# Kernel optimization log

Hardware: AMD Instinct MI355X
Metric: run time of the kernel (lower is better)

Reference implementation:

```python
import jax, jax.numpy as jnp
import numpy as np

N = 4096
E_EDGES = 262144
F_IN = 128      # num_features
H = 4           # nhead (GAT heads and MHA heads)
C = 64          # d_model (per-head GAT out dim)
EMB = H * C     # 256, MHA embed_dim
DFF = 128       # dim_feedforward
HD = EMB // H   # MHA head dim = 64


def setup_inputs() -> dict:
    key = jax.random.key(0)
    ks = jax.random.split(key, 16)
    inp = {}
    inp["tgt"] = jax.random.normal(ks[0], (N, F_IN), jnp.float32)
    inp["memory"] = jax.random.normal(ks[1], (N, EMB), jnp.float32)
    inp["original_signal"] = jax.random.normal(ks[2], (N, EMB), jnp.float32)
    inp["edge_index"] = jax.random.randint(ks[3], (2, E_EDGES), 0, N, jnp.int32)
    # GATConv params (PyG: lin has no bias; separate bias of size H*C; att vectors [1,H,C])
    s = 1.0 / np.sqrt(F_IN)
    inp["W_gat"] = jax.random.normal(ks[4], (F_IN, H * C), jnp.float32) * s
    inp["att_src"] = jax.random.normal(ks[5], (H, C), jnp.float32) * (1.0 / np.sqrt(C))
    inp["att_dst"] = jax.random.normal(ks[6], (H, C), jnp.float32) * (1.0 / np.sqrt(C))
    inp["b_gat"] = jnp.zeros((H * C,), jnp.float32)
    # nn.MultiheadAttention params
    se = 1.0 / np.sqrt(EMB)
    inp["in_proj_w"] = jax.random.normal(ks[7], (3 * EMB, EMB), jnp.float32) * se
    inp["in_proj_b"] = jnp.zeros((3 * EMB,), jnp.float32)
    inp["out_proj_w"] = jax.random.normal(ks[8], (EMB, EMB), jnp.float32) * se
    inp["out_proj_b"] = jnp.zeros((EMB,), jnp.float32)
    # linear1
    inp["lin1_w"] = jax.random.normal(ks[9], (DFF, EMB), jnp.float32) * se
    inp["lin1_b"] = jnp.zeros((DFF,), jnp.float32)
    return inp


def _gat_conv(x, edge_index, W, att_src, att_dst, bias):
    n = x.shape[0]
    xh = (x @ W).reshape(n, H, C)                       # [N,H,C]
    a_s = jnp.sum(xh * att_src, axis=-1)                # [N,H]
    a_d = jnp.sum(xh * att_dst, axis=-1)                # [N,H]
    # add self loops (PyG default add_self_loops=True)
    loop = jnp.arange(n, dtype=edge_index.dtype)
    src = jnp.concatenate([edge_index[0], loop])
    dst = jnp.concatenate([edge_index[1], loop])
    alpha = jax.nn.leaky_relu(a_s[src] + a_d[dst], negative_slope=0.2)  # [E+N,H]
    # edge softmax grouped by destination node
    m = jax.ops.segment_max(alpha, dst, num_segments=n)
    alpha = jnp.exp(alpha - m[dst])
    denom = jax.ops.segment_sum(alpha, dst, num_segments=n)
    alpha = alpha / (denom[dst] + 1e-16)
    # message passing: weighted scatter-add of source features
    out = jax.ops.segment_sum(xh[src] * alpha[:, :, None], dst, num_segments=n)  # [N,H,C]
    return out.reshape(n, H * C) + bias


def _mha(q_in, k_in, v_in, in_proj_w, in_proj_b, out_proj_w, out_proj_b):
    # batch=1, seq=N; dropout inactive (eval)
    q = q_in @ in_proj_w[:EMB].T + in_proj_b[:EMB]
    k = k_in @ in_proj_w[EMB:2 * EMB].T + in_proj_b[EMB:2 * EMB]
    v = v_in @ in_proj_w[2 * EMB:].T + in_proj_b[2 * EMB:]
    q = q.reshape(-1, H, HD)
    k = k.reshape(-1, H, HD)
    v = v.reshape(-1, H, HD)
    scale = 1.0 / np.sqrt(HD)
    scores = jnp.einsum('nhd,mhd->hnm', q * scale, k)   # [H,N,N]
    attn = jax.nn.softmax(scores, axis=-1)
    o = jnp.einsum('hnm,mhd->nhd', attn, v).reshape(-1, EMB)
    return o @ out_proj_w.T + out_proj_b


def reference(tgt, memory, original_signal, edge_index,
              W_gat, att_src, att_dst, b_gat,
              in_proj_w, in_proj_b, out_proj_w, out_proj_b,
              lin1_w, lin1_b):
    t = _gat_conv(tgt, edge_index, W_gat, att_src, att_dst, b_gat)
    t = jax.nn.leaky_relu(t, negative_slope=0.01)       # F.leaky_relu default slope
    fused = _mha(t, memory, original_signal, in_proj_w, in_proj_b, out_proj_w, out_proj_b)
    return jax.nn.relu(fused @ lin1_w.T + lin1_b)       # [N, DFF]
```

## Files before the change

kernel.cpp:

```cpp
#include <hip/hip_runtime.h>
#include <hip/hip_bf16.h>

#define NN   4096
#define EE   262144
#define ET   (EE + NN)
#define HH   4
#define EMB  256
#define DFF  128
#define FIN  128
#define KSPLIT 8
#define KCHUNK (NN / KSPLIT)

typedef float  f32x16  __attribute__((ext_vector_type(16)));
typedef __bf16 bf16x8  __attribute__((ext_vector_type(8)));
typedef unsigned short u16;
typedef unsigned short u16x4 __attribute__((ext_vector_type(4)));

__device__ __forceinline__ u16 f2bf(float f) {
  unsigned u = __float_as_uint(f);
  u += 0x7fffu + ((u >> 16) & 1u);
  return (u16)(u >> 16);
}
__device__ __forceinline__ unsigned split1(float x) {
  const u16 h = f2bf(x);
  const float hf = __uint_as_float(((unsigned)h) << 16);
  const u16 l = f2bf(x - hf);
  return (unsigned)h | ((unsigned)l << 16);
}

__global__ __launch_bounds__(256) void mgemm_nt(
    const float* __restrict__ A, const float* __restrict__ B,
    float* __restrict__ Cf, int M, int Nn, int K)
{
  __shared__ u16 Ah[64][40], Al[64][40], Bh[64][40], Bl[64][40];
  const int tid = threadIdx.x;
  const int m0 = blockIdx.y * 64, n0 = blockIdx.x * 64;
  const int w = tid >> 6, l = tid & 63, lq = l & 31, hi = l >> 5;
  const int wm = w >> 1, wn = w & 1;
  f32x16 acc = {0};
  for (int k0 = 0; k0 < K; k0 += 32) {
    __syncthreads();
#pragma unroll
    for (int it = 0; it < 2; ++it) {
      const int idx = tid + it * 256;
      {
        const int row = idx >> 3, slot = idx & 7;
        const float4 av = *(const float4*)(A + (size_t)(m0 + row) * K + k0 + slot * 4);
        const unsigned s0 = split1(av.x), s1 = split1(av.y), s2 = split1(av.z), s3 = split1(av.w);
        u16x4 hp = {(u16)s0, (u16)s1, (u16)s2, (u16)s3};
        u16x4 lp = {(u16)(s0 >> 16), (u16)(s1 >> 16), (u16)(s2 >> 16), (u16)(s3 >> 16)};
        *(u16x4*)(&Ah[row][slot * 4]) = hp;
        *(u16x4*)(&Al[row][slot * 4]) = lp;
      }
      {
        const int kr = idx >> 4, nq = idx & 15;
        const float4 bv = *(const float4*)(B + (size_t)(k0 + kr) * Nn + n0 + nq * 4);
        const unsigned s0 = split1(bv.x), s1 = split1(bv.y), s2 = split1(bv.z), s3 = split1(bv.w);
        Bh[nq * 4 + 0][kr] = (u16)s0; Bl[nq * 4 + 0][kr] = (u16)(s0 >> 16);
        Bh[nq * 4 + 1][kr] = (u16)s1; Bl[nq * 4 + 1][kr] = (u16)(s1 >> 16);
        Bh[nq * 4 + 2][kr] = (u16)s2; Bl[nq * 4 + 2][kr] = (u16)(s2 >> 16);
        Bh[nq * 4 + 3][kr] = (u16)s3; Bl[nq * 4 + 3][kr] = (u16)(s3 >> 16);
      }
    }
    __syncthreads();
#pragma unroll
    for (int c = 0; c < 2; ++c) {
      const bf16x8 ah = *(const bf16x8*)(&Ah[wm * 32 + lq][c * 16 + hi * 8]);
      const bf16x8 al = *(const bf16x8*)(&Al[wm * 32 + lq][c * 16 + hi * 8]);
      const bf16x8 bh = *(const bf16x8*)(&Bh[wn * 32 + lq][c * 16 + hi * 8]);
      const bf16x8 bl = *(const bf16x8*)(&Bl[wn * 32 + lq][c * 16 + hi * 8]);
      acc = __builtin_amdgcn_mfma_f32_32x32x16_bf16(ah, bh, acc, 0, 0, 0);
      acc = __builtin_amdgcn_mfma_f32_32x32x16_bf16(ah, bl, acc, 0, 0, 0);
      acc = __builtin_amdgcn_mfma_f32_32x32x16_bf16(al, bh, acc, 0, 0, 0);
    }
  }
  const int col = n0 + wn * 32 + lq;
#pragma unroll
  for (int r = 0; r < 16; ++r) {
    const int row = m0 + wm * 32 + (r & 3) + 8 * (r >> 2) + 4 * hi;
    Cf[(size_t)row * Nn + col] = acc[r];
  }
}

__global__ __launch_bounds__(256) void bgemm(
    const float* __restrict__ A, const float* __restrict__ B, const float* __restrict__ bias,
    float* __restrict__ Cf, int M, int Nn, int K, int act)
{
  __shared__ u16 As[64][40], Bs[64][40];
  const int tid = threadIdx.x;
  const int m0 = blockIdx.y * 64, n0 = blockIdx.x * 64;
  const int w = tid >> 6, l = tid & 63, lq = l & 31, hi = l >> 5;
  const int wm = w >> 1, wn = w & 1;
  f32x16 acc = {0};
  for (int k0 = 0; k0 < K; k0 += 32) {
    __syncthreads();
#pragma unroll
    for (int it = 0; it < 2; ++it) {
      const int idx = tid + it * 256;
      const int row = idx >> 3, slot = idx & 7;
      const float4 av = *(const float4*)(A + (size_t)(m0 + row) * K + k0 + slot * 4);
      u16x4 ap = {f2bf(av.x), f2bf(av.y), f2bf(av.z), f2bf(av.w)};
      *(u16x4*)(&As[row][slot * 4]) = ap;
      const float4 bv = *(const float4*)(B + (size_t)(n0 + row) * K + k0 + slot * 4);
      u16x4 bp = {f2bf(bv.x), f2bf(bv.y), f2bf(bv.z), f2bf(bv.w)};
      *(u16x4*)(&Bs[row][slot * 4]) = bp;
    }
    __syncthreads();
#pragma unroll
    for (int c = 0; c < 2; ++c) {
      const bf16x8 af = *(const bf16x8*)(&As[wm * 32 + lq][c * 16 + hi * 8]);
      const bf16x8 bf = *(const bf16x8*)(&Bs[wn * 32 + lq][c * 16 + hi * 8]);
      acc = __builtin_amdgcn_mfma_f32_32x32x16_bf16(af, bf, acc, 0, 0, 0);
    }
  }
  const int col = n0 + wn * 32 + lq;
  const float bcol = bias ? bias[col] : 0.f;
#pragma unroll
  for (int r = 0; r < 16; ++r) {
    const int row = m0 + wm * 32 + (r & 3) + 8 * (r >> 2) + 4 * hi;
    float v = acc[r] + bcol;
    if (act == 2) v = fmaxf(v, 0.f);
    Cf[(size_t)row * Nn + col] = v;
  }
}

__global__ __launch_bounds__(256) void qkv_mfma(
    const float* __restrict__ tbuf, const float* __restrict__ mem, const float* __restrict__ orig,
    const float* __restrict__ ipw, const float* __restrict__ ipb,
    u16* __restrict__ qb, u16* __restrict__ kbuf, u16* __restrict__ vT)
{
  __shared__ u16 As[64][40], Bs[64][40];
  const int z = blockIdx.z;
  const float* A = (z == 0) ? tbuf : (z == 1 ? mem : orig);
  const float* B = ipw + (size_t)z * EMB * EMB;
  const float* bias = ipb + z * EMB;
  const float oscale = (z == 0) ? 0.125f : 1.f;
  const int tid = threadIdx.x;
  const int m0 = blockIdx.y * 64, n0 = blockIdx.x * 64;
  const int w = tid >> 6, l = tid & 63, lq = l & 31, hi = l >> 5;
  const int wm = w >> 1, wn = w & 1;
  f32x16 acc = {0};
  for (int k0 = 0; k0 < EMB; k0 += 32) {
    __syncthreads();
#pragma unroll
    for (int it = 0; it < 2; ++it) {
      const int idx = tid + it * 256;
      const int row = idx >> 3, slot = idx & 7;
      const float4 av = *(const float4*)(A + (size_t)(m0 + row) * EMB + k0 + slot * 4);
      u16x4 ap = {f2bf(av.x), f2bf(av.y), f2bf(av.z), f2bf(av.w)};
      *(u16x4*)(&As[row][slot * 4]) = ap;
      const float4 bv = *(const float4*)(B + (size_t)(n0 + row) * EMB + k0 + slot * 4);
      u16x4 bp = {f2bf(bv.x), f2bf(bv.y), f2bf(bv.z), f2bf(bv.w)};
      *(u16x4*)(&Bs[row][slot * 4]) = bp;
    }
    __syncthreads();
#pragma unroll
    for (int c = 0; c < 2; ++c) {
      const bf16x8 af = *(const bf16x8*)(&As[wm * 32 + lq][c * 16 + hi * 8]);
      const bf16x8 bf = *(const bf16x8*)(&Bs[wn * 32 + lq][c * 16 + hi * 8]);
      acc = __builtin_amdgcn_mfma_f32_32x32x16_bf16(af, bf, acc, 0, 0, 0);
    }
  }
  const int col = n0 + wn * 32 + lq;
  const float bcol = bias[col];
  const int hh = col >> 6, dd = col & 63;
#pragma unroll
  for (int r = 0; r < 16; ++r) {
    const int row = m0 + wm * 32 + (r & 3) + 8 * (r >> 2) + 4 * hi;
    const u16 bw = f2bf((acc[r] + bcol) * oscale);
    if (z == 2) vT[((size_t)hh * 64 + dd) * NN + row] = bw;
    else if (z == 1) kbuf[((size_t)hh * NN + row) * 64 + dd] = bw;
    else qb[((size_t)hh * NN + row) * 64 + dd] = bw;
  }
}

__global__ __launch_bounds__(256) void att_sums(const float* __restrict__ xh,
                                                const float* __restrict__ att_src,
                                                const float* __restrict__ att_dst,
                                                float* __restrict__ a_s, float* __restrict__ a_d)
{
  const int n = blockIdx.x, t = threadIdx.x;
  const int h = t >> 6, c = t & 63;
  const float v = xh[(size_t)n * EMB + t];
  float s1 = v * att_src[t];
  float s2 = v * att_dst[t];
#pragma unroll
  for (int off = 32; off >= 1; off >>= 1) {
    s1 += __shfl_down(s1, off);
    s2 += __shfl_down(s2, off);
  }
  if (c == 0) { a_s[n * HH + h] = s1; a_d[n * HH + h] = s2; }
}

__global__ void edge_count(const int* __restrict__ ei, int* __restrict__ counts) {
  const int e = blockIdx.x * blockDim.x + threadIdx.x;
  if (e >= ET) return;
  const int dst = (e < EE) ? ei[EE + e] : (e - EE);
  atomicAdd(&counts[dst], 1);
}

__global__ __launch_bounds__(64) void scan4096(const int* __restrict__ counts, int* __restrict__ offs) {
  const int t = threadIdx.x;
  const int base = t * 64;
  int s = 0;
  for (int i = 0; i < 64; ++i) s += counts[base + i];
  int incl = s;
#pragma unroll
  for (int off = 1; off < 64; off <<= 1) {
    const int v = __shfl_up(incl, off);
    if (t >= off) incl += v;
  }
  int run = incl - s;
  for (int i = 0; i < 64; ++i) { offs[base + i] = run; run += counts[base + i]; }
}

__global__ void edge_scatter(const int* __restrict__ ei, const int* __restrict__ offs,
                             int* __restrict__ cursor, int* __restrict__ ssrc) {
  const int e = blockIdx.x * blockDim.x + threadIdx.x;
  if (e >= ET) return;
  int src, dst;
  if (e < EE) { src = ei[e]; dst = ei[EE + e]; } else { src = dst = e - EE; }
  const int pos = offs[dst] + atomicAdd(&cursor[dst], 1);
  ssrc[pos] = src;
}

__global__ __launch_bounds__(256) void gat_gather(
    const float* __restrict__ xh, const float* __restrict__ a_s, const float* __restrict__ a_d,
    const int* __restrict__ offs, const int* __restrict__ counts, const int* __restrict__ ssrc,
    const float* __restrict__ b_gat, float* __restrict__ t_out)
{
  const int dst = blockIdx.x, tid = threadIdx.x;
  const int h = tid >> 6, c = tid & 63;
  const float ad = a_d[dst * HH + h];
  const int beg = offs[dst], deg = counts[dst];
  float ac0 = 0.f, ac1 = 0.f, ac2 = 0.f, ac3 = 0.f;
  float dn0 = 0.f, dn1 = 0.f, dn2 = 0.f, dn3 = 0.f;
  int i = 0;
  for (; i + 4 <= deg; i += 4) {
    const int s0 = ssrc[beg + i];
    const int s1 = ssrc[beg + i + 1];
    const int s2 = ssrc[beg + i + 2];
    const int s3 = ssrc[beg + i + 3];
    const float A0 = a_s[s0 * HH + h];
    const float A1 = a_s[s1 * HH + h];
    const float A2 = a_s[s2 * HH + h];
    const float A3 = a_s[s3 * HH + h];
    const float x0 = xh[(size_t)s0 * EMB + h * 64 + c];
    const float x1 = xh[(size_t)s1 * EMB + h * 64 + c];
    const float x2 = xh[(size_t)s2 * EMB + h * 64 + c];
    const float x3 = xh[(size_t)s3 * EMB + h * 64 + c];
    float a0 = A0 + ad; a0 = a0 > 0.f ? a0 : 0.2f * a0;
    float a1 = A1 + ad; a1 = a1 > 0.f ? a1 : 0.2f * a1;
    float a2 = A2 + ad; a2 = a2 > 0.f ? a2 : 0.2f * a2;
    float a3 = A3 + ad; a3 = a3 > 0.f ? a3 : 0.2f * a3;
    const float p0 = __expf(a0);
    const float p1 = __expf(a1);
    const float p2 = __expf(a2);
    const float p3 = __expf(a3);
    dn0 += p0; ac0 += p0 * x0;
    dn1 += p1; ac1 += p1 * x1;
    dn2 += p2; ac2 += p2 * x2;
    dn3 += p3; ac3 += p3 * x3;
  }
  for (; i < deg; ++i) {
    const int src = ssrc[beg + i];
    float a = a_s[src * HH + h] + ad;
    a = a > 0.f ? a : 0.2f * a;
    const float p = __expf(a);
    dn0 += p;
    ac0 += p * xh[(size_t)src * EMB + h * 64 + c];
  }
  const float den = (dn0 + dn1) + (dn2 + dn3);
  const float accv = (ac0 + ac1) + (ac2 + ac3);
  float v = accv / (den + 1e-16f) + b_gat[tid];
  v = v > 0.f ? v : 0.01f * v;
  t_out[(size_t)dst * EMB + tid] = v;
}

__global__ __launch_bounds__(256) void flash32(
    const u16* __restrict__ qb, const u16* __restrict__ kb,
    const u16* __restrict__ vT, float* __restrict__ po,
    float* __restrict__ pm, float* __restrict__ pl)
{
  __shared__ float sld[4][32 * 33];
  const int h = blockIdx.y;
  const int qgroup = blockIdx.x / KSPLIT, ks = blockIdx.x % KSPLIT;
  const int w = threadIdx.x >> 6, l = threadIdx.x & 63;
  const int lq = l & 31, hi = l >> 5;
  const int qtile = qgroup * 4 + w;
  const int q0 = qtile * 32;
  const u16* qh = qb + (size_t)h * NN * 64;
  const u16* kh = kb + (size_t)h * NN * 64;
  const u16* vh = vT + (size_t)h * 64 * NN;

  bf16x8 qf[4];
#pragma unroll
  for (int c = 0; c < 4; ++c)
    qf[c] = *(const bf16x8*)(qh + (size_t)(q0 + lq) * 64 + c * 16 + hi * 8);

  f32x16 o0 = {0}, o1 = {0};
  float m_r = -1e30f, l_r = 0.f;

  const int kend = ks * KCHUNK + KCHUNK;
  for (int k0 = ks * KCHUNK; k0 < kend; k0 += 32) {
    f32x16 s = {0};
#pragma unroll
    for (int c = 0; c < 4; ++c) {
      const bf16x8 kf = *(const bf16x8*)(kh + (size_t)(k0 + lq) * 64 + c * 16 + hi * 8);
      s = __builtin_amdgcn_mfma_f32_32x32x16_bf16(kf, qf[c], s, 0, 0, 0);
    }
    float mx = s[0];
#pragma unroll
    for (int i = 1; i < 16; ++i) mx = fmaxf(mx, s[i]);
    const float colmax = fmaxf(mx, __shfl_xor(mx, 32));
    if (!__all(colmax <= m_r + 8.f)) {
      const float m_new = fmaxf(m_r, colmax);
      const float corr = __expf(m_r - m_new);
#pragma unroll
      for (int i = 0; i < 16; ++i) { o0[i] *= corr; o1[i] *= corr; }
      l_r *= corr;
      m_r = m_new;
    }
    float p[16];
    float ssum = 0.f;
#pragma unroll
    for (int i = 0; i < 16; ++i) { p[i] = __expf(s[i] - m_r); ssum += p[i]; }
    l_r += ssum + __shfl_xor(ssum, 32);

    unsigned wd[8];
#pragma unroll
    for (int i = 0; i < 8; ++i)
      wd[i] = (unsigned)f2bf(p[2 * i]) | ((unsigned)f2bf(p[2 * i + 1]) << 16);
    const unsigned t0 = __shfl_xor(hi ? wd[0] : wd[2], 32);
    const unsigned t1 = __shfl_xor(hi ? wd[1] : wd[3], 32);
    const unsigned t2 = __shfl_xor(hi ? wd[4] : wd[6], 32);
    const unsigned t3 = __shfl_xor(hi ? wd[5] : wd[7], 32);
    union { unsigned u[4]; bf16x8 b; } pf0, pf1;
    pf0.u[0] = hi ? t0 : wd[0];
    pf0.u[1] = hi ? t1 : wd[1];
    pf0.u[2] = hi ? wd[2] : t0;
    pf0.u[3] = hi ? wd[3] : t1;
    pf1.u[0] = hi ? t2 : wd[4];
    pf1.u[1] = hi ? t3 : wd[5];
    pf1.u[2] = hi ? wd[6] : t2;
    pf1.u[3] = hi ? wd[7] : t3;
    {
      const u16* vrow = vh + (size_t)lq * NN + k0 + hi * 8;
      const bf16x8 vf0 = *(const bf16x8*)(vrow);
      const bf16x8 vf1 = *(const bf16x8*)(vrow + 16);
      o0 = __builtin_amdgcn_mfma_f32_32x32x16_bf16(vf0, pf0.b, o0, 0, 0, 0);
      o0 = __builtin_amdgcn_mfma_f32_32x32x16_bf16(vf1, pf1.b, o0, 0, 0, 0);
    }
    {
      const u16* vrow = vh + (size_t)(32 + lq) * NN + k0 + hi * 8;
      const bf16x8 vf0 = *(const bf16x8*)(vrow);
      const bf16x8 vf1 = *(const bf16x8*)(vrow + 16);
      o1 = __builtin_amdgcn_mfma_f32_32x32x16_bf16(vf0, pf0.b, o1, 0, 0, 0);
      o1 = __builtin_amdgcn_mfma_f32_32x32x16_bf16(vf1, pf1.b, o1, 0, 0, 0);
    }
  }

  float* wld = sld[w];
  const size_t rowbase = (size_t)h * NN + q0;
  const int qq2 = (l >> 5), dd = l & 31;
#pragma unroll
  for (int r = 0; r < 16; ++r)
    wld[((r & 3) + 8 * (r >> 2) + 4 * hi) * 33 + lq] = o0[r];
#pragma unroll
  for (int qi = 0; qi < 16; ++qi) {
    const int qr = qi * 2 + qq2;
    po[(rowbase + qr) * (KSPLIT * 64) + ks * 64 + dd] = wld[dd * 33 + qr];
  }
#pragma unroll
  for (int r = 0; r < 16; ++r)
    wld[((r & 3) + 8 * (r >> 2) + 4 * hi) * 33 + lq] = o1[r];
#pragma unroll
  for (int qi = 0; qi < 16; ++qi) {
    const int qr = qi * 2 + qq2;
    po[(rowbase + qr) * (KSPLIT * 64) + ks * 64 + 32 + dd] = wld[dd * 33 + qr];
  }
  if (hi == 0) {
    const int pidx = (h * KSPLIT + ks) * NN + q0 + lq;
    pm[pidx] = m_r; pl[pidx] = l_r;
  }
}

__global__ __launch_bounds__(256) void combine2(
    const float* __restrict__ po, const float* __restrict__ pm,
    const float* __restrict__ pl, float* __restrict__ o)
{
  const int q = blockIdx.x;
  const int t = threadIdx.x;
  const int h = t >> 6, d = t & 63;
  float mloc[KSPLIT];
  float M = -1e30f;
#pragma unroll
  for (int i = 0; i < KSPLIT; ++i) {
    mloc[i] = pm[(h * KSPLIT + i) * NN + q];
    M = fmaxf(M, mloc[i]);
  }
  const size_t base = ((size_t)h * NN + q) * (KSPLIT * 64);
  float L = 0.f, acc = 0.f;
#pragma unroll
  for (int i = 0; i < KSPLIT; ++i) {
    const float wgt = __expf(mloc[i] - M);
    L += wgt * pl[(h * KSPLIT + i) * NN + q];
    acc += wgt * po[base + i * 64 + d];
  }
  o[(size_t)q * EMB + h * 64 + d] = acc / L;
}

extern "C" void kernel_launch(void* const* d_in, const int* in_sizes, int n_in,
                              void* d_out, int out_size, void* d_ws, size_t ws_size,
                              hipStream_t stream)
{
  const float* tgt   = (const float*)d_in[0];
  const float* mem   = (const float*)d_in[1];
  const float* orig  = (const float*)d_in[2];
  const int*   eidx  = (const int*)d_in[3];
  const float* Wg    = (const float*)d_in[4];
  const float* att_s = (const float*)d_in[5];
  const float* att_d = (const float*)d_in[6];
  const float* bg    = (const float*)d_in[7];
  const float* ipw   = (const float*)d_in[8];
  const float* ipb   = (const float*)d_in[9];
  const float* opw   = (const float*)d_in[10];
  const float* opb   = (const float*)d_in[11];
  const float* l1w   = (const float*)d_in[12];
  const float* l1b   = (const float*)d_in[13];
  float* out = (float*)d_out;

  char* ws = (char*)d_ws;
  size_t off = 0;
  auto alloc = [&](size_t bytes) -> void* {
    void* p = ws + off;
    off += (bytes + 255) & ~((size_t)255);
    return p;
  };
  float* xh    = (float*)alloc((size_t)NN * EMB * 4);
  float* tbuf  = (float*)alloc((size_t)NN * EMB * 4);
  float* a_s   = (float*)alloc((size_t)NN * HH * 4);
  float* a_d   = (float*)alloc((size_t)NN * HH * 4);
  int* counts  = (int*)alloc((size_t)NN * 4);
  int* offs    = (int*)alloc((size_t)NN * 4);
  int* cursor  = (int*)alloc((size_t)NN * 4);
  int* ssrc    = (int*)alloc((size_t)ET * 4);
  u16* qb      = (u16*)alloc((size_t)NN * EMB * 2);
  u16* kbuf    = (u16*)alloc((size_t)NN * EMB * 2);
  u16* vT      = (u16*)alloc((size_t)NN * EMB * 2);
  float* po    = (float*)alloc((size_t)HH * NN * KSPLIT * 64 * 4);
  float* pm    = (float*)alloc((size_t)HH * KSPLIT * NN * 4);
  float* pl    = (float*)alloc((size_t)HH * KSPLIT * NN * 4);
  float* obuf  = xh;
  float* fused = tbuf;

  (void)hipMemsetAsync(counts, 0, (size_t)NN * 4, stream);
  (void)hipMemsetAsync(cursor, 0, (size_t)NN * 4, stream);

  mgemm_nt<<<dim3(EMB / 64, NN / 64), 256, 0, stream>>>(tgt, Wg, xh, NN, EMB, FIN);
  att_sums<<<NN, 256, 0, stream>>>(xh, att_s, att_d, a_s, a_d);
  edge_count<<<(ET + 255) / 256, 256, 0, stream>>>(eidx, counts);
  scan4096<<<1, 64, 0, stream>>>(counts, offs);
  edge_scatter<<<(ET + 255) / 256, 256, 0, stream>>>(eidx, offs, cursor, ssrc);
  gat_gather<<<NN, 256, 0, stream>>>(xh, a_s, a_d, offs, counts, ssrc, bg, tbuf);

  qkv_mfma<<<dim3(EMB / 64, NN / 64, 3), 256, 0, stream>>>(
      tbuf, mem, orig, ipw, ipb, qb, kbuf, vT);

  flash32<<<dim3(32 * KSPLIT, HH), 256, 0, stream>>>(qb, kbuf, vT, po, pm, pl);
  combine2<<<NN, 256, 0, stream>>>(po, pm, pl, obuf);

  bgemm<<<dim3(EMB / 64, NN / 64), 256, 0, stream>>>(
      obuf, opw, opb, fused, NN, EMB, EMB, 0);
  bgemm<<<dim3(DFF / 64, NN / 64), 256, 0, stream>>>(
      fused, l1w, l1b, out, NN, DFF, EMB, 2);
}
```

Baseline: 210.5 us.

## Stage V tiles via global_load_lds and drop edge cursor buffer

In the flash attention kernel, the V operand is now loaded with global-to-LDS direct loads issued at the top of each key-tile iteration. The loads are read back from LDS after the QK/softmax work, so their latency is meant to overlap the score computation. The edge scatter now atomically bumps the offsets array itself instead of a separate cursor, and the gather recovers each start as offs minus degree. This removes a memset and a buffer, but it adds an LDS buffer per wave and a full vmcnt(0) wait inside the loop.

```diff
diff --git a/kernel.cpp b/kernel.cpp
--- a/kernel.cpp
+++ b/kernel.cpp
@@ -214,13 +214,13 @@
   for (int i = 0; i < 64; ++i) { offs[base + i] = run; run += counts[base + i]; }
 }
 
-__global__ void edge_scatter(const int* __restrict__ ei, const int* __restrict__ offs,
-                             int* __restrict__ cursor, int* __restrict__ ssrc) {
+__global__ void edge_scatter(const int* __restrict__ ei, int* __restrict__ offs,
+                             int* __restrict__ ssrc) {
   const int e = blockIdx.x * blockDim.x + threadIdx.x;
   if (e >= ET) return;
   int src, dst;
   if (e < EE) { src = ei[e]; dst = ei[EE + e]; } else { src = dst = e - EE; }
-  const int pos = offs[dst] + atomicAdd(&cursor[dst], 1);
+  const int pos = atomicAdd(&offs[dst], 1);
   ssrc[pos] = src;
 }
 
@@ -232,7 +232,8 @@
   const int dst = blockIdx.x, tid = threadIdx.x;
   const int h = tid >> 6, c = tid & 63;
   const float ad = a_d[dst * HH + h];
-  const int beg = offs[dst], deg = counts[dst];
+  const int deg = counts[dst];
+  const int beg = offs[dst] - deg;
   float ac0 = 0.f, ac1 = 0.f, ac2 = 0.f, ac3 = 0.f;
   float dn0 = 0.f, dn1 = 0.f, dn2 = 0.f, dn3 = 0.f;
   int i = 0;
@@ -283,6 +284,7 @@
     float* __restrict__ pm, float* __restrict__ pl)
 {
   __shared__ float sld[4][32 * 33];
+  __shared__ u16 vbuf[4][4 * 512];
   const int h = blockIdx.y;
   const int qgroup = blockIdx.x / KSPLIT, ks = blockIdx.x % KSPLIT;
   const int w = threadIdx.x >> 6, l = threadIdx.x & 63;
@@ -303,6 +305,21 @@
 
   const int kend = ks * KCHUNK + KCHUNK;
   for (int k0 = ks * KCHUNK; k0 < kend; k0 += 32) {
+    {
+      const u16* g0 = vh + (size_t)lq * NN + k0 + hi * 8;
+      const u16* g1 = vh + (size_t)lq * NN + k0 + hi * 8 + 16;
+      const u16* g2 = vh + (size_t)(32 + lq) * NN + k0 + hi * 8;
+      const u16* g3 = vh + (size_t)(32 + lq) * NN + k0 + hi * 8 + 16;
+      __builtin_amdgcn_global_load_lds((const __attribute__((address_space(1))) unsigned*)g0,
+                                       (__attribute__((address_space(3))) unsigned*)&vbuf[w][0 * 512], 16, 0, 0);
+      __builtin_amdgcn_global_load_lds((const __attribute__((address_space(1))) unsigned*)g1,
+                                       (__attribute__((address_space(3))) unsigned*)&vbuf[w][1 * 512], 16, 0, 0);
+      __builtin_amdgcn_global_load_lds((const __attribute__((address_space(1))) unsigned*)g2,
+                                       (__attribute__((address_space(3))) unsigned*)&vbuf[w][2 * 512], 16, 0, 0);
+      __builtin_amdgcn_global_load_lds((const __attribute__((address_space(1))) unsigned*)g3,
+                                       (__attribute__((address_space(3))) unsigned*)&vbuf[w][3 * 512], 16, 0, 0);
+    }
+
     f32x16 s = {0};
 #pragma unroll
     for (int c = 0; c < 4; ++c) {
@@ -344,20 +361,16 @@
     pf1.u[1] = hi ? t3 : wd[5];
     pf1.u[2] = hi ? wd[6] : t2;
     pf1.u[3] = hi ? wd[7] : t3;
-    {
-      const u16* vrow = vh + (size_t)lq * NN + k0 + hi * 8;
-      const bf16x8 vf0 = *(const bf16x8*)(vrow);
-      const bf16x8 vf1 = *(const bf16x8*)(vrow + 16);
-      o0 = __builtin_amdgcn_mfma_f32_32x32x16_bf16(vf0, pf0.b, o0, 0, 0, 0);
-      o0 = __builtin_amdgcn_mfma_f32_32x32x16_bf16(vf1, pf1.b, o0, 0, 0, 0);
-    }
-    {
-      const u16* vrow = vh + (size_t)(32 + lq) * NN + k0 + hi * 8;
-      const bf16x8 vf0 = *(const bf16x8*)(vrow);
-      const bf16x8 vf1 = *(const bf16x8*)(vrow + 16);
-      o1 = __builtin_amdgcn_mfma_f32_32x32x16_bf16(vf0, pf0.b, o1, 0, 0, 0);
-      o1 = __builtin_amdgcn_mfma_f32_32x32x16_bf16(vf1, pf1.b, o1, 0, 0, 0);
-    }
+
+    asm volatile("s_waitcnt vmcnt(0)" ::: "memory");
+    const bf16x8 vf00 = *(const bf16x8*)(&vbuf[w][0 * 512 + l * 8]);
+    const bf16x8 vf01 = *(const bf16x8*)(&vbuf[w][1 * 512 + l * 8]);
+    const bf16x8 vf10 = *(const bf16x8*)(&vbuf[w][2 * 512 + l * 8]);
+    const bf16x8 vf11 = *(const bf16x8*)(&vbuf[w][3 * 512 + l * 8]);
+    o0 = __builtin_amdgcn_mfma_f32_32x32x16_bf16(vf00, pf0.b, o0, 0, 0, 0);
+    o1 = __builtin_amdgcn_mfma_f32_32x32x16_bf16(vf10, pf0.b, o1, 0, 0, 0);
+    o0 = __builtin_amdgcn_mfma_f32_32x32x16_bf16(vf01, pf1.b, o0, 0, 0, 0);
+    o1 = __builtin_amdgcn_mfma_f32_32x32x16_bf16(vf11, pf1.b, o1, 0, 0, 0);
   }
 
   float* wld = sld[w];
@@ -443,7 +456,6 @@
   float* a_d   = (float*)alloc((size_t)NN * HH * 4);
   int* counts  = (int*)alloc((size_t)NN * 4);
   int* offs    = (int*)alloc((size_t)NN * 4);
-  int* cursor  = (int*)alloc((size_t)NN * 4);
   int* ssrc    = (int*)alloc((size_t)ET * 4);
   u16* qb      = (u16*)alloc((size_t)NN * EMB * 2);
   u16* kbuf    = (u16*)alloc((size_t)NN * EMB * 2);
@@ -455,13 +467,12 @@
   float* fused = tbuf;
 
   (void)hipMemsetAsync(counts, 0, (size_t)NN * 4, stream);
-  (void)hipMemsetAsync(cursor, 0, (size_t)NN * 4, stream);
 
   mgemm_nt<<<dim3(EMB / 64, NN / 64), 256, 0, stream>>>(tgt, Wg, xh, NN, EMB, FIN);
   att_sums<<<NN, 256, 0, stream>>>(xh, att_s, att_d, a_s, a_d);
   edge_count<<<(ET + 255) / 256, 256, 0, stream>>>(eidx, counts);
   scan4096<<<1, 64, 0, stream>>>(counts, offs);
-  edge_scatter<<<(ET + 255) / 256, 256, 0, stream>>>(eidx, offs, cursor, ssrc);
+  edge_scatter<<<(ET + 255) / 256, 256, 0, stream>>>(eidx, offs, ssrc);
   gat_gather<<<NN, 256, 0, stream>>>(xh, a_s, a_d, offs, counts, ssrc, bg, tbuf);
 
   qkv_mfma<<<dim3(EMB / 64, NN / 64, 3), 256, 0, stream>>>(
```

Result: slower. 222.1 us (+5.5%).
